# Kernel tuning notes

Measured on AMD Instinct MI355X. Metric: run time of the kernel, lower is better.

The kernel has to match this reference:

```python
import jax, jax.numpy as jnp
import numpy as np

B, S = 2, 1024          # 2 sequences of 1024 tokens (prefill)
HID = 2880
HQ, HKV, D = 64, 8, 64  # query heads, kv heads, head_dim
W = 128                 # sliding window size
THETA = 150000.0
SCALE = D ** -0.5
Q_SIZE, KV_SIZE = HQ * D, HKV * D


def _rope_neox(pos, x):
    # pos: [T] int, x: [T, H, D] -> neox-style full-dim rotary
    half = D // 2
    inv_freq = 1.0 / (THETA ** (jnp.arange(half, dtype=jnp.float32) * 2.0 / D))
    ang = pos.astype(jnp.float32)[:, None] * inv_freq          # [T, D/2]
    cos = jnp.cos(ang)[:, None, :]                             # [T, 1, D/2]
    sin = jnp.sin(ang)[:, None, :]
    x1, x2 = x[..., :half], x[..., half:]
    return jnp.concatenate([x1 * cos - x2 * sin, x1 * sin + x2 * cos], axis=-1)


def setup_inputs() -> dict:
    key = jax.random.key(0)
    ks = jax.random.split(key, 10)
    s = 0.02
    hidden_states = jax.random.normal(ks[0], (B * S, HID), dtype=jnp.float32)
    positions = jnp.tile(jnp.arange(S, dtype=jnp.int32), B)    # per-sequence positions
    Wq = jax.random.normal(ks[1], (HID, Q_SIZE), dtype=jnp.float32) * s
    bq = jax.random.normal(ks[2], (Q_SIZE,), dtype=jnp.float32) * s
    Wk = jax.random.normal(ks[3], (HID, KV_SIZE), dtype=jnp.float32) * s
    bk = jax.random.normal(ks[4], (KV_SIZE,), dtype=jnp.float32) * s
    Wv = jax.random.normal(ks[5], (HID, KV_SIZE), dtype=jnp.float32) * s
    bv = jax.random.normal(ks[6], (KV_SIZE,), dtype=jnp.float32) * s
    Wo = jax.random.normal(ks[7], (Q_SIZE, HID), dtype=jnp.float32) * s
    bo = jax.random.normal(ks[8], (HID,), dtype=jnp.float32) * s
    return {"hidden_states": hidden_states, "positions": positions,
            "Wq": Wq, "bq": bq, "Wk": Wk, "bk": bk,
            "Wv": Wv, "bv": bv, "Wo": Wo, "bo": bo}


def reference(hidden_states, positions, Wq, bq, Wk, bk, Wv, bv, Wo, bo):
    T = hidden_states.shape[0]
    q = (hidden_states @ Wq + bq).reshape(T, HQ, D)
    k = (hidden_states @ Wk + bk).reshape(T, HKV, D)
    v = (hidden_states @ Wv + bv).reshape(T, HKV, D)
    q = _rope_neox(positions, q)
    k = _rope_neox(positions, k)

    # sliding-window causal attention (banded, window = last W keys + self)
    G = HQ // HKV  # GQA group size
    q5 = q.reshape(B, S, HKV, G, D)
    k4 = k.reshape(B, S, HKV, D)
    v4 = v.reshape(B, S, HKV, D)
    offs = jnp.arange(W + 1)
    idx = jnp.arange(S)[:, None] - W + offs[None, :]           # [S, W+1] key index j
    valid = idx >= 0                                           # causal+window band
    idx_c = jnp.clip(idx, 0, S - 1)
    kw = k4[:, idx_c]                                          # [B, S, W+1, HKV, D]
    vw = v4[:, idx_c]
    scores = jnp.einsum('bikgd,biwkd->bikgw', q5, kw) * SCALE  # [B,S,HKV,G,W+1]
    scores = jnp.where(valid[None, :, None, None, :], scores, jnp.float32(-1e30))
    p = jax.nn.softmax(scores, axis=-1)
    o = jnp.einsum('bikgw,biwkd->bikgd', p, vw).reshape(T, Q_SIZE)
    return o @ Wo + bo


if __name__ == '__main__':
    out = reference(**setup_inputs())
    print(out.shape, out.dtype)
```

## Files before the change

kernel.cpp:

```cpp
#include <hip/hip_runtime.h>

#define T_TOK 2048
#define S_LEN 1024
#define HIDN  2880
#define NHQ   64
#define NHKV  8
#define DH    64
#define QSZ   4096
#define KVSZ  512
#define WIN   128
#define NQKV  5120
#define NOPAD 2944
#define NT    45

typedef __attribute__((ext_vector_type(4))) float f32x4;
typedef __attribute__((ext_vector_type(8))) short bf16x8;
typedef __attribute__((ext_vector_type(4))) short s16x4;

__device__ __forceinline__ unsigned short f2bf(float f) {
  unsigned u = __float_as_uint(f);
  u += 0x7fffu + ((u >> 16) & 1u);
  return (unsigned short)(u >> 16);
}
__device__ __forceinline__ float bf2f(unsigned short s) {
  return __uint_as_float(((unsigned)s) << 16);
}
__device__ __forceinline__ void ld_g2l16(const void* g, void* l) {
  __builtin_amdgcn_global_load_lds(
      (const __attribute__((address_space(1))) unsigned int*)g,
      (__attribute__((address_space(3))) unsigned int*)l, 16, 0, 0);
}

#define NB_CONV 2880
#define NB_WQ   5760
#define NB_WK   720

__device__ __forceinline__ void transpose_tile(
    const float* __restrict__ W, unsigned short* __restrict__ WT,
    int N, int lbid, float (*tile)[72])
{
  const int tid = threadIdx.x;
  const int nbx = N >> 6;
  const int nb = (lbid % nbx) * 64;
  const int kb = (lbid / nbx) * 32;
  const int kk = tid >> 3;
  const int n8 = (tid & 7) * 8;
  const float* src = W + (size_t)(kb + kk) * N + nb + n8;
  *(f32x4*)&tile[kk][n8]     = *(const f32x4*)(src);
  *(f32x4*)&tile[kk][n8 + 4] = *(const f32x4*)(src + 4);
  __syncthreads();
  const int n  = tid & 63;
  const int k8 = (tid >> 6) * 8;
  bf16x8 p;
  #pragma unroll
  for (int j = 0; j < 8; ++j) p[j] = (short)f2bf(tile[k8 + j][n]);
  *(bf16x8*)(WT + (size_t)(nb + n) * HIDN + kb + k8) = p;
}

__global__ __launch_bounds__(256) void prep_kernel(
    const float* __restrict__ hidden, unsigned short* __restrict__ hbf,
    const float* __restrict__ Wq, const float* __restrict__ Wk,
    const float* __restrict__ Wv, unsigned short* __restrict__ WT)
{
  __shared__ float tile[32][72];
  const int bid = blockIdx.x;
  if (bid < NB_CONV) {
    const size_t off = ((size_t)bid * 256 + threadIdx.x) * 8;
    const f32x4 a = *(const f32x4*)(hidden + off);
    const f32x4 b = *(const f32x4*)(hidden + off + 4);
    bf16x8 p;
    p[0] = (short)f2bf(a[0]); p[1] = (short)f2bf(a[1]);
    p[2] = (short)f2bf(a[2]); p[3] = (short)f2bf(a[3]);
    p[4] = (short)f2bf(b[0]); p[5] = (short)f2bf(b[1]);
    p[6] = (short)f2bf(b[2]); p[7] = (short)f2bf(b[3]);
    *(bf16x8*)(hbf + off) = p;
  } else if (bid < NB_CONV + NB_WQ) {
    transpose_tile(Wq, WT, QSZ, bid - NB_CONV, tile);
  } else if (bid < NB_CONV + NB_WQ + NB_WK) {
    transpose_tile(Wk, WT + (size_t)QSZ * HIDN, KVSZ,
                   bid - NB_CONV - NB_WQ, tile);
  } else {
    transpose_tile(Wv, WT + (size_t)(QSZ + KVSZ) * HIDN, KVSZ,
                   bid - NB_CONV - NB_WQ - NB_WK, tile);
  }
}

__global__ __launch_bounds__(256) void transpose_w(
    const float* __restrict__ W, unsigned short* __restrict__ WT,
    int K, int N)
{
  __shared__ float tile[32][72];
  const int tid = threadIdx.x;
  const int nb = blockIdx.x * 64;
  const int kb = blockIdx.y * 32;
  const int kk = tid >> 3;
  const int n8 = (tid & 7) * 8;
  if (nb + 64 <= N) {
    const float* src = W + (size_t)(kb + kk) * N + nb + n8;
    *(f32x4*)&tile[kk][n8]     = *(const f32x4*)(src);
    *(f32x4*)&tile[kk][n8 + 4] = *(const f32x4*)(src + 4);
  } else {
    #pragma unroll
    for (int u = 0; u < 8; ++u)
      tile[kk][n8 + u] = (nb + n8 + u < N)
          ? W[(size_t)(kb + kk) * N + nb + n8 + u] : 0.f;
  }
  __syncthreads();
  const int n  = tid & 63;
  const int k8 = (tid >> 6) * 8;
  bf16x8 p;
  #pragma unroll
  for (int j = 0; j < 8; ++j) p[j] = (short)f2bf(tile[k8 + j][n]);
  *(bf16x8*)(WT + (size_t)(nb + n) * K + kb + k8) = p;
}

__device__ __forceinline__ void rope_epilogue8(
    f32x4 (*acc)[4], const float* __restrict__ bias,
    const int* __restrict__ pos, unsigned short* __restrict__ outp,
    int outStride, int colbase, int rowbase, int lane)
{
  const int fr = lane & 15;
  const int r4 = (lane >> 4) * 4;
  const float invf0 = exp2f((float)fr        * (-17.19460283f / 32.0f));
  const float invf1 = exp2f((float)(fr + 16) * (-17.19460283f / 32.0f));
  #pragma unroll
  for (int mt = 0; mt < 8; ++mt) {
    #pragma unroll
    for (int i = 0; i < 4; ++i) {
      const int m = rowbase + mt * 16 + r4 + i;
      const float p = (float)pos[m];
      #pragma unroll
      for (int ntp = 0; ntp < 2; ++ntp) {
        float sv, cv;
        __sincosf(p * (ntp ? invf1 : invf0), &sv, &cv);
        const int c1 = colbase + ntp * 16 + fr;
        const float x1 = acc[mt][ntp][i]     + bias[c1];
        const float x2 = acc[mt][ntp + 2][i] + bias[c1 + 32];
        outp[(size_t)m * outStride + c1]      = f2bf(x1 * cv - x2 * sv);
        outp[(size_t)m * outStride + c1 + 32] = f2bf(x1 * sv + x2 * cv);
      }
    }
  }
}

__global__ __launch_bounds__(512, 2) void gemm_qkv(
    const unsigned short* __restrict__ A, const unsigned short* __restrict__ BT,
    const float* __restrict__ bq, const float* __restrict__ bk,
    const float* __restrict__ bv, const int* __restrict__ pos,
    unsigned short* __restrict__ qb, unsigned short* __restrict__ kb,
    unsigned short* __restrict__ vT)
{
  __shared__ unsigned short lds[65536];
  const int tid  = threadIdx.x;
  const int lane = tid & 63;
  const int wid  = tid >> 6;
  const int wm   = wid >> 2;
  const int wn   = wid & 3;
  const int bid  = blockIdx.x;
  const int wg   = (bid & 7) * 20 + (bid >> 3);
  const int n0   = (wg % 20) * 256;
  const int m0   = (wg / 20) * 256;
  const int fr = lane & 15;
  const int fq = lane >> 4;

  const int rsub = tid >> 3;
  const int cg   = (tid & 7) ^ (rsub & 7);
  const unsigned short* Asrc = A  + (size_t)(m0 + rsub) * HIDN + cg * 8;
  const unsigned short* Bsrc = BT + (size_t)(n0 + rsub) * HIDN + cg * 8;
  const size_t half_step = (size_t)128 * HIDN;
  const size_t r64 = (size_t)64 * HIDN;

  #define STAGE(src, slot)                                         \
    do {                                                           \
      ld_g2l16((src),       (slot) + (size_t)tid * 8);             \
      ld_g2l16((src) + r64, (slot) + (size_t)(512 + tid) * 8);     \
    } while (0)

  STAGE(Bsrc,                  lds + 16384);
  STAGE(Bsrc + half_step,      lds + 24576);
  STAGE(Asrc,                  lds + 0);
  STAGE(Asrc + half_step,      lds + 8192);
  STAGE(Bsrc + 64,             lds + 32768 + 16384);
  STAGE(Bsrc + half_step + 64, lds + 32768 + 24576);
  STAGE(Asrc + 64,             lds + 32768 + 0);
  STAGE(Asrc + half_step + 64, lds + 32768 + 8192);
  asm volatile("s_waitcnt vmcnt(8)" ::: "memory");
  __builtin_amdgcn_s_barrier();

  f32x4 acc[8][4];
  #pragma unroll
  for (int i = 0; i < 8; ++i)
    #pragma unroll
    for (int j = 0; j < 4; ++j) acc[i][j] = (f32x4){0.f, 0.f, 0.f, 0.f};
  bf16x8 bfr[4][2];

  for (int t = 0; t < NT; ++t) {
    unsigned short* Abuf = lds + (t & 1) * 32768;
    unsigned short* Bbuf = Abuf + 16384;
    unsigned short* nAbuf = lds + ((t + 1) & 1) * 32768;
    const int kA = (t + 1) * 64;
    const int kB = (t + 2) * 64;
    #pragma unroll
    for (int q = 0; q < 4; ++q) {
      if (q == 0) {
        #pragma unroll
        for (int nf = 0; nf < 4; ++nf)
          #pragma unroll
          for (int ks = 0; ks < 2; ++ks) {
            const int R = wn * 64 + nf * 16 + fr;
            const int kc = ks * 4 + fq;
            bfr[nf][ks] = *(const bf16x8*)(Bbuf + R * 64 + ((kc ^ (R & 7)) << 3));
          }
      }
      bf16x8 af[2][2];
      #pragma unroll
      for (int j = 0; j < 2; ++j)
        #pragma unroll
        for (int ks = 0; ks < 2; ++ks) {
          const int R = wm * 128 + (q * 2 + j) * 16 + fr;
          const int kc = ks * 4 + fq;
          af[j][ks] = *(const bf16x8*)(Abuf + R * 64 + ((kc ^ (R & 7)) << 3));
        }
      if (q == 0) {
        if (t >= 1 && t <= NT - 2) STAGE(Asrc + kA, nAbuf);
      } else if (q == 1) {
        if (t >= 1 && t <= NT - 2) STAGE(Asrc + half_step + kA, nAbuf + 8192);
      } else if (q == 2) {
        if (t <= NT - 3) STAGE(Bsrc + kB, Bbuf);
      } else {
        if (t <= NT - 3) STAGE(Bsrc + half_step + kB, Bbuf + 8192);
      }
      if (q == 3) {
        if (t < NT - 2)       asm volatile("s_waitcnt vmcnt(4)" ::: "memory");
        else if (t == NT - 2) asm volatile("s_waitcnt vmcnt(0)" ::: "memory");
      }
      __builtin_amdgcn_s_barrier();
      __builtin_amdgcn_s_setprio(1);
      #pragma unroll
      for (int j = 0; j < 2; ++j)
        #pragma unroll
        for (int nf = 0; nf < 4; ++nf)
          #pragma unroll
          for (int ks = 0; ks < 2; ++ks)
            acc[q * 2 + j][nf] = __builtin_amdgcn_mfma_f32_16x16x32_bf16(
                af[j][ks], bfr[nf][ks], acc[q * 2 + j][nf], 0, 0, 0);
      __builtin_amdgcn_s_setprio(0);
      __builtin_amdgcn_s_barrier();
    }
  }
  #undef STAGE

  const int cb = n0 + wn * 64;
  const int rowbase = m0 + wm * 128;
  if (cb < QSZ) {
    rope_epilogue8(acc, bq, pos, qb, QSZ, cb, rowbase, lane);
  } else if (cb < QSZ + KVSZ) {
    rope_epilogue8(acc, bk, pos, kb, KVSZ, cb - QSZ, rowbase, lane);
  } else {
    const int r4 = (lane >> 4) * 4;
    #pragma unroll
    for (int nt = 0; nt < 4; ++nt) {
      const int vrow = cb - (QSZ + KVSZ) + nt * 16 + fr;
      const float bvv = bv[vrow];
      #pragma unroll
      for (int mt = 0; mt < 8; ++mt) {
        const int mb = rowbase + mt * 16 + r4;
        s16x4 p;
        p[0] = (short)f2bf(acc[mt][nt][0] + bvv);
        p[1] = (short)f2bf(acc[mt][nt][1] + bvv);
        p[2] = (short)f2bf(acc[mt][nt][2] + bvv);
        p[3] = (short)f2bf(acc[mt][nt][3] + bvv);
        *(s16x4*)(vT + (size_t)vrow * T_TOK + mb) = p;
      }
    }
  }
}

__global__ __launch_bounds__(256) void gemm_o(
    const unsigned short* __restrict__ A, const unsigned short* __restrict__ BT,
    const float* __restrict__ bias, float* __restrict__ C)
{
  __shared__ unsigned short As[128 * 64];
  __shared__ unsigned short Bs[128 * 64];
  const int tid  = threadIdx.x;
  const int lane = tid & 63;
  const int wid  = tid >> 6;
  const int wr   = (wid >> 1) * 64;
  const int wc   = (wid & 1) * 64;
  const int m0 = blockIdx.y * 128;
  const int n0 = blockIdx.x * 128;
  const int fr = lane & 15;
  const int fq = lane >> 4;

  f32x4 acc[4][4];
  #pragma unroll
  for (int i = 0; i < 4; ++i)
    #pragma unroll
    for (int j = 0; j < 4; ++j) acc[i][j] = (f32x4){0.f, 0.f, 0.f, 0.f};

  const int rsub = tid >> 3;
  const int cg   = (tid & 7) ^ (rsub & 7);
  const unsigned short* Ap = A  + (size_t)(m0 + rsub) * QSZ + cg * 8;
  const unsigned short* Bp = BT + (size_t)(n0 + rsub) * QSZ + cg * 8;
  const size_t rstep = (size_t)32 * QSZ;

  for (int k0 = 0; k0 < QSZ; k0 += 64) {
    #pragma unroll
    for (int i = 0; i < 4; ++i)
      ld_g2l16(Ap + i * rstep + k0, As + ((size_t)i * 256 + tid) * 8);
    #pragma unroll
    for (int i = 0; i < 4; ++i)
      ld_g2l16(Bp + i * rstep + k0, Bs + ((size_t)i * 256 + tid) * 8);
    __syncthreads();
    #pragma unroll
    for (int ks = 0; ks < 2; ++ks) {
      const int kc = ks * 4 + fq;
      bf16x8 af[4], bfr[4];
      #pragma unroll
      for (int mt = 0; mt < 4; ++mt) {
        const int R = wr + mt * 16 + fr;
        af[mt] = *(const bf16x8*)(As + R * 64 + ((kc ^ (R & 7)) << 3));
      }
      #pragma unroll
      for (int nt = 0; nt < 4; ++nt) {
        const int R = wc + nt * 16 + fr;
        bfr[nt] = *(const bf16x8*)(Bs + R * 64 + ((kc ^ (R & 7)) << 3));
      }
      #pragma unroll
      for (int mt = 0; mt < 4; ++mt)
        #pragma unroll
        for (int nt = 0; nt < 4; ++nt)
          acc[mt][nt] = __builtin_amdgcn_mfma_f32_16x16x32_bf16(
              af[mt], bfr[nt], acc[mt][nt], 0, 0, 0);
    }
    __syncthreads();
  }

  const int r4 = (lane >> 4) * 4;
  #pragma unroll
  for (int nt = 0; nt < 4; ++nt) {
    const int n = n0 + wc + nt * 16 + fr;
    if (n >= HIDN) continue;
    const float bvv = bias[n];
    #pragma unroll
    for (int mt = 0; mt < 4; ++mt) {
      const int mb = m0 + wr + mt * 16 + r4;
      #pragma unroll
      for (int i = 0; i < 4; ++i)
        C[(size_t)(mb + i) * HIDN + n] = acc[mt][nt][i] + bvv;
    }
  }
}

__global__ __launch_bounds__(256, 3) void attn_kernel(
    const unsigned short* __restrict__ q, const unsigned short* __restrict__ k,
    const unsigned short* __restrict__ vT, unsigned short* __restrict__ o)
{
  __shared__ unsigned short lds[26624];
  unsigned short* Ks = lds;
  unsigned short* Vt = lds;
  unsigned short* Ps = lds + 13824;

  const int tid  = threadIdx.x;
  const int lane = tid & 63;
  const int wid  = tid >> 6;
  const int sq0  = blockIdx.x * 64;
  const int hp   = blockIdx.y;
  const int b    = blockIdx.z;
  const int h0   = hp * 2;
  const int kvh  = hp >> 2;
  const int kp0  = sq0 - WIN;

  const int fr = lane & 15;
  const int fk = (lane >> 4) * 8;
  const int qw = wid * 16;

  bf16x8 qf[2][2];
  {
    const size_t qrow = (size_t)(b * S_LEN + sq0 + qw + fr) * QSZ;
    #pragma unroll
    for (int hh = 0; hh < 2; ++hh)
      #pragma unroll
      for (int ks2 = 0; ks2 < 2; ++ks2)
        qf[hh][ks2] = *(const bf16x8*)(q + qrow + (h0 + hh) * DH + ks2 * 32 + fk);
  }

  #pragma unroll
  for (int j = 0; j < 6; ++j) {
    const int c  = tid + j * 256;
    const int kr = c >> 3, dc = (c & 7) * 8;
    int tok = b * S_LEN + kp0 + kr;
    if (tok < 0) tok = 0;
    const bf16x8 vv = *(const bf16x8*)(k + (size_t)tok * KVSZ + kvh * DH + dc);
    *(bf16x8*)&Ks[kr * 72 + dc] = vv;
  }
  __syncthreads();

  f32x4 S0[12], S1[12];
  #pragma unroll
  for (int i = 0; i < 12; ++i) {
    S0[i] = (f32x4){0.f, 0.f, 0.f, 0.f};
    S1[i] = (f32x4){0.f, 0.f, 0.f, 0.f};
  }
  #pragma unroll
  for (int ks2 = 0; ks2 < 2; ++ks2) {
    #pragma unroll
    for (int nt = 0; nt < 12; ++nt) {
      const bf16x8 bfr = *(const bf16x8*)&Ks[(nt * 16 + fr) * 72 + ks2 * 32 + fk];
      S0[nt] = __builtin_amdgcn_mfma_f32_16x16x32_bf16(qf[0][ks2], bfr, S0[nt], 0, 0, 0);
      S1[nt] = __builtin_amdgcn_mfma_f32_16x16x32_bf16(qf[1][ks2], bfr, S1[nt], 0, 0, 0);
    }
  }

  const int qbase = sq0 + qw + ((lane >> 4) << 2);
  float ls0[4] = {0.f, 0.f, 0.f, 0.f};
  float ls1[4] = {0.f, 0.f, 0.f, 0.f};
  #pragma unroll
  for (int nt = 0; nt < 12; ++nt) {
    const int jpos = kp0 + nt * 16 + fr;
    #pragma unroll
    for (int i = 0; i < 4; ++i) {
      const int qa = qbase + i;
      const bool valid = (jpos >= 0) && (jpos <= qa) && (jpos >= qa - WIN);
      const float e0 = valid ? __expf(S0[nt][i] * 0.125f) : 0.f;
      const float e1 = valid ? __expf(S1[nt][i] * 0.125f) : 0.f;
      S0[nt][i] = e0; ls0[i] += e0;
      S1[nt][i] = e1; ls1[i] += e1;
    }
  }
  #pragma unroll
  for (int off = 1; off < 16; off <<= 1)
    #pragma unroll
    for (int i = 0; i < 4; ++i) {
      ls0[i] += __shfl_xor(ls0[i], off, 64);
      ls1[i] += __shfl_xor(ls1[i], off, 64);
    }
  float inv0[4], inv1[4];
  #pragma unroll
  for (int i = 0; i < 4; ++i) {
    inv0[i] = 1.0f / ls0[i];
    inv1[i] = 1.0f / ls1[i];
  }
  __syncthreads();

  #pragma unroll
  for (int nt = 0; nt < 12; ++nt)
    #pragma unroll
    for (int i = 0; i < 4; ++i)
      Ps[(qbase - sq0 + i) * 200 + nt * 16 + fr] = f2bf(S0[nt][i]);
  if (kp0 >= 0) {
    #pragma unroll
    for (int j = 0; j < 6; ++j) {
      const int c  = tid + j * 256;
      const int dr = c / 24, kc = (c % 24) * 8;
      const bf16x8 vv = *(const bf16x8*)(
          vT + (size_t)(kvh * DH + dr) * T_TOK + b * S_LEN + kp0 + kc);
      *(bf16x8*)&Vt[dr * 200 + kc] = vv;
    }
  } else {
    #pragma unroll
    for (int j = 0; j < 6; ++j) {
      const int c  = tid + j * 256;
      const int dr = c / 24, kc = (c % 24) * 8;
      bf16x8 vv;
      #pragma unroll
      for (int u = 0; u < 8; ++u) {
        int col = b * S_LEN + kp0 + kc + u;
        if (col < 0) col = 0;
        vv[u] = (short)vT[(size_t)(kvh * DH + dr) * T_TOK + col];
      }
      *(bf16x8*)&Vt[dr * 200 + kc] = vv;
    }
  }
  __syncthreads();

  {
    f32x4 O[4];
    #pragma unroll
    for (int i = 0; i < 4; ++i) O[i] = (f32x4){0.f, 0.f, 0.f, 0.f};
    #pragma unroll
    for (int ks2 = 0; ks2 < 6; ++ks2) {
      const bf16x8 pa = *(const bf16x8*)&Ps[(qw + fr) * 200 + ks2 * 32 + fk];
      #pragma unroll
      for (int nt = 0; nt < 4; ++nt) {
        const bf16x8 vb = *(const bf16x8*)&Vt[(nt * 16 + fr) * 200 + ks2 * 32 + fk];
        O[nt] = __builtin_amdgcn_mfma_f32_16x16x32_bf16(pa, vb, O[nt], 0, 0, 0);
      }
    }
    #pragma unroll
    for (int nt = 0; nt < 4; ++nt)
      #pragma unroll
      for (int i = 0; i < 4; ++i)
        o[(size_t)(b * S_LEN + qbase + i) * QSZ + h0 * DH + nt * 16 + fr] =
            f2bf(O[nt][i] * inv0[i]);
  }
  __syncthreads();

  #pragma unroll
  for (int nt = 0; nt < 12; ++nt)
    #pragma unroll
    for (int i = 0; i < 4; ++i)
      Ps[(qbase - sq0 + i) * 200 + nt * 16 + fr] = f2bf(S1[nt][i]);
  __syncthreads();

  {
    f32x4 O[4];
    #pragma unroll
    for (int i = 0; i < 4; ++i) O[i] = (f32x4){0.f, 0.f, 0.f, 0.f};
    #pragma unroll
    for (int ks2 = 0; ks2 < 6; ++ks2) {
      const bf16x8 pa = *(const bf16x8*)&Ps[(qw + fr) * 200 + ks2 * 32 + fk];
      #pragma unroll
      for (int nt = 0; nt < 4; ++nt) {
        const bf16x8 vb = *(const bf16x8*)&Vt[(nt * 16 + fr) * 200 + ks2 * 32 + fk];
        O[nt] = __builtin_amdgcn_mfma_f32_16x16x32_bf16(pa, vb, O[nt], 0, 0, 0);
      }
    }
    #pragma unroll
    for (int nt = 0; nt < 4; ++nt)
      #pragma unroll
      for (int i = 0; i < 4; ++i)
        o[(size_t)(b * S_LEN + qbase + i) * QSZ + (h0 + 1) * DH + nt * 16 + fr] =
            f2bf(O[nt][i] * inv1[i]);
  }
}

extern "C" void kernel_launch(void* const* d_in, const int* in_sizes, int n_in,
                              void* d_out, int out_size, void* d_ws, size_t ws_size,
                              hipStream_t stream) {
  const float* hidden    = (const float*)d_in[0];
  const int*   positions = (const int*)d_in[1];
  const float* Wq = (const float*)d_in[2];
  const float* bq = (const float*)d_in[3];
  const float* Wk = (const float*)d_in[4];
  const float* bk = (const float*)d_in[5];
  const float* Wv = (const float*)d_in[6];
  const float* bv = (const float*)d_in[7];
  const float* Wo = (const float*)d_in[8];
  const float* bo = (const float*)d_in[9];
  float* out = (float*)d_out;

  char* ws = (char*)d_ws;
  unsigned short* hbf   = (unsigned short*)(ws);
  unsigned short* WqkvT = (unsigned short*)(ws + 11796480);
  unsigned short* qb    = (unsigned short*)(ws + 41287680);
  unsigned short* kb    = (unsigned short*)(ws + 58064896);
  unsigned short* vTb   = (unsigned short*)(ws + 60162048);

  prep_kernel<<<dim3(NB_CONV + NB_WQ + 2 * NB_WK), dim3(256), 0, stream>>>(
      hidden, hbf, Wq, Wk, Wv, WqkvT);

  gemm_qkv<<<dim3((NQKV / 256) * (T_TOK / 256)), dim3(512), 0, stream>>>(
      hbf, WqkvT, bq, bk, bv, positions, qb, kb, vTb);

  transpose_w<<<dim3(NOPAD / 64, QSZ / 32), dim3(256), 0, stream>>>(
      Wo, WqkvT, QSZ, HIDN);

  attn_kernel<<<dim3(S_LEN / 64, NHQ / 2, 2), dim3(256), 0, stream>>>(
      qb, kb, vTb, qb);
  gemm_o<<<dim3(NOPAD / 128, T_TOK / 128), dim3(256), 0, stream>>>(
      qb, WqkvT, bo, out);
}
```

Baseline: 359.4 us.

## Pipeline output GEMM with double-buffered LDS and merge Wo transpose into QKV launch

The output projection GEMM is rewritten to use 512-thread blocks on 256x128 tiles. It double-buffers LDS with async global-to-LDS prefetch, splits the MFMA work into two phases bracketed by barriers and priority hints, and remaps blocks for locality. The Wo transpose-to-bf16 work moves into extra blocks of the QKV GEMM launch when the workspace is large enough. This lets it overlap the GEMM tail and removes a separate launch. It adds scheduling complexity and depends on the workspace size check.

```diff
diff --git a/kernel.cpp b/kernel.cpp
--- a/kernel.cpp
+++ b/kernel.cpp
@@ -12,6 +12,7 @@
 #define NQKV  5120
 #define NOPAD 2944
 #define NT    45
+#define NTO   64
 
 typedef __attribute__((ext_vector_type(4))) float f32x4;
 typedef __attribute__((ext_vector_type(8))) short bf16x8;
@@ -148,15 +149,46 @@
     const float* __restrict__ bq, const float* __restrict__ bk,
     const float* __restrict__ bv, const int* __restrict__ pos,
     unsigned short* __restrict__ qb, unsigned short* __restrict__ kb,
-    unsigned short* __restrict__ vT)
+    unsigned short* __restrict__ vT,
+    const float* __restrict__ Wo, unsigned short* __restrict__ WoT)
 {
   __shared__ unsigned short lds[65536];
   const int tid  = threadIdx.x;
+  const int bid  = blockIdx.x;
+
+  if (bid >= 160) {
+    const int t2   = (bid - 160) * 2 + (tid >> 8);
+    const int ltid = tid & 255;
+    float* fb = (float*)lds;
+    float (*tile)[72] = (float (*)[72])(fb + (tid >> 8) * (32 * 72));
+    const int nb = (t2 % 46) * 64;
+    const int kb = (t2 / 46) * 32;
+    const int kk = ltid >> 3;
+    const int n8 = (ltid & 7) * 8;
+    if (nb + 64 <= HIDN) {
+      const float* src = Wo + (size_t)(kb + kk) * HIDN + nb + n8;
+      *(f32x4*)&tile[kk][n8]     = *(const f32x4*)(src);
+      *(f32x4*)&tile[kk][n8 + 4] = *(const f32x4*)(src + 4);
+    } else {
+      #pragma unroll
+      for (int u = 0; u < 8; ++u)
+        tile[kk][n8 + u] = (nb + n8 + u < HIDN)
+            ? Wo[(size_t)(kb + kk) * HIDN + nb + n8 + u] : 0.f;
+    }
+    __syncthreads();
+    const int n  = ltid & 63;
+    const int k8 = (ltid >> 6) * 8;
+    bf16x8 p;
+    #pragma unroll
+    for (int j = 0; j < 8; ++j) p[j] = (short)f2bf(tile[k8 + j][n]);
+    *(bf16x8*)(WoT + (size_t)(nb + n) * QSZ + kb + k8) = p;
+    return;
+  }
+
   const int lane = tid & 63;
   const int wid  = tid >> 6;
   const int wm   = wid >> 2;
   const int wn   = wid & 3;
-  const int bid  = blockIdx.x;
   const int wg   = (bid & 7) * 20 + (bid >> 3);
   const int n0   = (wg % 20) * 256;
   const int m0   = (wg / 20) * 256;
@@ -276,75 +308,119 @@
   }
 }
 
-__global__ __launch_bounds__(256) void gemm_o(
+__global__ __launch_bounds__(512, 2) void gemm_o(
     const unsigned short* __restrict__ A, const unsigned short* __restrict__ BT,
     const float* __restrict__ bias, float* __restrict__ C)
 {
-  __shared__ unsigned short As[128 * 64];
-  __shared__ unsigned short Bs[128 * 64];
+  __shared__ unsigned short lds[49152];
   const int tid  = threadIdx.x;
   const int lane = tid & 63;
   const int wid  = tid >> 6;
-  const int wr   = (wid >> 1) * 64;
-  const int wc   = (wid & 1) * 64;
-  const int m0 = blockIdx.y * 128;
-  const int n0 = blockIdx.x * 128;
+  const int wm   = wid >> 1;
+  const int wn   = wid & 1;
+  const int bid  = blockIdx.x;
+  const int wg   = (bid & 7) * 23 + (bid >> 3);
+  const int m0   = (wg / 23) * 256;
+  const int n0   = (wg % 23) * 128;
   const int fr = lane & 15;
   const int fq = lane >> 4;
 
-  f32x4 acc[4][4];
-  #pragma unroll
-  for (int i = 0; i < 4; ++i)
-    #pragma unroll
-    for (int j = 0; j < 4; ++j) acc[i][j] = (f32x4){0.f, 0.f, 0.f, 0.f};
-
   const int rsub = tid >> 3;
   const int cg   = (tid & 7) ^ (rsub & 7);
-  const unsigned short* Ap = A  + (size_t)(m0 + rsub) * QSZ + cg * 8;
-  const unsigned short* Bp = BT + (size_t)(n0 + rsub) * QSZ + cg * 8;
-  const size_t rstep = (size_t)32 * QSZ;
-
-  for (int k0 = 0; k0 < QSZ; k0 += 64) {
-    #pragma unroll
-    for (int i = 0; i < 4; ++i)
-      ld_g2l16(Ap + i * rstep + k0, As + ((size_t)i * 256 + tid) * 8);
-    #pragma unroll
-    for (int i = 0; i < 4; ++i)
-      ld_g2l16(Bp + i * rstep + k0, Bs + ((size_t)i * 256 + tid) * 8);
-    __syncthreads();
-    #pragma unroll
-    for (int ks = 0; ks < 2; ++ks) {
-      const int kc = ks * 4 + fq;
-      bf16x8 af[4], bfr[4];
-      #pragma unroll
-      for (int mt = 0; mt < 4; ++mt) {
-        const int R = wr + mt * 16 + fr;
-        af[mt] = *(const bf16x8*)(As + R * 64 + ((kc ^ (R & 7)) << 3));
-      }
-      #pragma unroll
-      for (int nt = 0; nt < 4; ++nt) {
-        const int R = wc + nt * 16 + fr;
-        bfr[nt] = *(const bf16x8*)(Bs + R * 64 + ((kc ^ (R & 7)) << 3));
-      }
-      #pragma unroll
-      for (int mt = 0; mt < 4; ++mt)
+  const unsigned short* Asrc = A  + (size_t)(m0 + rsub) * QSZ + cg * 8;
+  const unsigned short* Bsrc = BT + (size_t)(n0 + rsub) * QSZ + cg * 8;
+  const size_t r64 = (size_t)64 * QSZ;
+
+  #define STA(t, r)  ld_g2l16(Asrc + (size_t)(t) * 64 + (size_t)(r) * r64,   \
+      lds + ((t) & 1) * 24576 + ((size_t)(r) * 512 + tid) * 8)
+  #define STB(t, r)  ld_g2l16(Bsrc + (size_t)(t) * 64 + (size_t)(r) * r64,   \
+      lds + ((t) & 1) * 24576 + 16384 + ((size_t)(r) * 512 + tid) * 8)
+
+  STB(0, 0); STB(0, 1);
+  STA(0, 0); STA(0, 1); STA(0, 2); STA(0, 3);
+  STB(1, 0); STB(1, 1);
+  STA(1, 0); STA(1, 1); STA(1, 2); STA(1, 3);
+  asm volatile("s_waitcnt vmcnt(6)" ::: "memory");
+  __builtin_amdgcn_s_barrier();
+
+  f32x4 acc[4][4];
+  #pragma unroll
+  for (int i = 0; i < 4; ++i)
+    #pragma unroll
+    for (int j = 0; j < 4; ++j) acc[i][j] = (f32x4){0.f, 0.f, 0.f, 0.f};
+  bf16x8 bfr[4][2];
+
+  for (int t = 0; t < NTO; ++t) {
+    unsigned short* Abuf = lds + (t & 1) * 24576;
+    unsigned short* Bbuf = Abuf + 16384;
+    #pragma unroll
+    for (int nf = 0; nf < 4; ++nf)
+      #pragma unroll
+      for (int ks = 0; ks < 2; ++ks) {
+        const int R = wn * 64 + nf * 16 + fr;
+        const int kc = ks * 4 + fq;
+        bfr[nf][ks] = *(const bf16x8*)(Bbuf + R * 64 + ((kc ^ (R & 7)) << 3));
+      }
+    bf16x8 af0[2][2];
+    #pragma unroll
+    for (int j = 0; j < 2; ++j)
+      #pragma unroll
+      for (int ks = 0; ks < 2; ++ks) {
+        const int R = wm * 64 + j * 16 + fr;
+        const int kc = ks * 4 + fq;
+        af0[j][ks] = *(const bf16x8*)(Abuf + R * 64 + ((kc ^ (R & 7)) << 3));
+      }
+    if (t >= 1 && t <= NTO - 2) { STA(t + 1, 0); STA(t + 1, 1); STA(t + 1, 2); }
+    __builtin_amdgcn_s_barrier();
+    __builtin_amdgcn_s_setprio(1);
+    #pragma unroll
+    for (int j = 0; j < 2; ++j)
+      #pragma unroll
+      for (int nf = 0; nf < 4; ++nf)
         #pragma unroll
-        for (int nt = 0; nt < 4; ++nt)
-          acc[mt][nt] = __builtin_amdgcn_mfma_f32_16x16x32_bf16(
-              af[mt], bfr[nt], acc[mt][nt], 0, 0, 0);
-    }
-    __syncthreads();
-  }
+        for (int ks = 0; ks < 2; ++ks)
+          acc[j][nf] = __builtin_amdgcn_mfma_f32_16x16x32_bf16(
+              af0[j][ks], bfr[nf][ks], acc[j][nf], 0, 0, 0);
+    __builtin_amdgcn_s_setprio(0);
+    __builtin_amdgcn_s_barrier();
+    bf16x8 af1[2][2];
+    #pragma unroll
+    for (int j = 0; j < 2; ++j)
+      #pragma unroll
+      for (int ks = 0; ks < 2; ++ks) {
+        const int R = wm * 64 + (2 + j) * 16 + fr;
+        const int kc = ks * 4 + fq;
+        af1[j][ks] = *(const bf16x8*)(Abuf + R * 64 + ((kc ^ (R & 7)) << 3));
+      }
+    if (t >= 1 && t <= NTO - 2) STA(t + 1, 3);
+    if (t <= NTO - 3) { STB(t + 2, 0); STB(t + 2, 1); }
+    if (t < NTO - 2)       asm volatile("s_waitcnt vmcnt(2)" ::: "memory");
+    else if (t == NTO - 2) asm volatile("s_waitcnt vmcnt(0)" ::: "memory");
+    __builtin_amdgcn_s_barrier();
+    __builtin_amdgcn_s_setprio(1);
+    #pragma unroll
+    for (int j = 0; j < 2; ++j)
+      #pragma unroll
+      for (int nf = 0; nf < 4; ++nf)
+        #pragma unroll
+        for (int ks = 0; ks < 2; ++ks)
+          acc[2 + j][nf] = __builtin_amdgcn_mfma_f32_16x16x32_bf16(
+              af1[j][ks], bfr[nf][ks], acc[2 + j][nf], 0, 0, 0);
+    __builtin_amdgcn_s_setprio(0);
+    __builtin_amdgcn_s_barrier();
+  }
+  #undef STA
+  #undef STB
 
   const int r4 = (lane >> 4) * 4;
   #pragma unroll
   for (int nt = 0; nt < 4; ++nt) {
-    const int n = n0 + wc + nt * 16 + fr;
+    const int n = n0 + wn * 64 + nt * 16 + fr;
     if (n >= HIDN) continue;
     const float bvv = bias[n];
     #pragma unroll
     for (int mt = 0; mt < 4; ++mt) {
-      const int mb = m0 + wr + mt * 16 + r4;
+      const int mb = m0 + wm * 64 + mt * 16 + r4;
       #pragma unroll
       for (int i = 0; i < 4; ++i)
         C[(size_t)(mb + i) * HIDN + n] = acc[mt][nt][i] + bvv;
@@ -547,17 +623,24 @@
   unsigned short* kb    = (unsigned short*)(ws + 58064896);
   unsigned short* vTb   = (unsigned short*)(ws + 60162048);
 
+  const bool merged = ws_size >= (size_t)86376448;
+  unsigned short* WoT = merged ? (unsigned short*)(ws + 62259200) : WqkvT;
+
   prep_kernel<<<dim3(NB_CONV + NB_WQ + 2 * NB_WK), dim3(256), 0, stream>>>(
       hidden, hbf, Wq, Wk, Wv, WqkvT);
 
-  gemm_qkv<<<dim3((NQKV / 256) * (T_TOK / 256)), dim3(512), 0, stream>>>(
-      hbf, WqkvT, bq, bk, bv, positions, qb, kb, vTb);
-
-  transpose_w<<<dim3(NOPAD / 64, QSZ / 32), dim3(256), 0, stream>>>(
-      Wo, WqkvT, QSZ, HIDN);
+  if (merged) {
+    gemm_qkv<<<dim3(160 + 2944), dim3(512), 0, stream>>>(
+        hbf, WqkvT, bq, bk, bv, positions, qb, kb, vTb, Wo, WoT);
+  } else {
+    gemm_qkv<<<dim3(160), dim3(512), 0, stream>>>(
+        hbf, WqkvT, bq, bk, bv, positions, qb, kb, vTb, Wo, WoT);
+    transpose_w<<<dim3(NOPAD / 64, QSZ / 32), dim3(256), 0, stream>>>(
+        Wo, WqkvT, QSZ, HIDN);
+  }
 
   attn_kernel<<<dim3(S_LEN / 64, NHQ / 2, 2), dim3(256), 0, stream>>>(
       qb, kb, vTb, qb);
-  gemm_o<<<dim3(NOPAD / 128, T_TOK / 128), dim3(256), 0, stream>>>(
-      qb, WqkvT, bo, out);
-}
+  gemm_o<<<dim3(184), dim3(512), 0, stream>>>(
+      qb, WoT, bo, out);
+}
```

Result: faster. 342.9 us (-4.6%).
